# Optimization experiments

Hardware: AMD Instinct MI355X
Metric: run time of the kernel (lower is better)

Reference implementation:

```python
import jax, jax.numpy as jnp
import numpy as np

TV, B, V = 2048, 16, 1024
TK, K = 2048, 1024


def setup_inputs() -> dict:
    key = jax.random.key(0)
    k1, k2, k3 = jax.random.split(key, 3)
    values = jax.random.normal(k1, (TV, B, V), dtype=jnp.float32)          # time-major values
    values_mask = jnp.ones((B, TV), dtype=jnp.int32)                        # unused by math, kept for fidelity
    keys = jax.random.normal(k2, (B, TK, K), dtype=jnp.float32)
    # xavier-normal-scaled projection weight (created inside torch forward)
    w = jax.random.normal(k3, (K, V), dtype=jnp.float32) * jnp.sqrt(2.0 / (K + V))
    return {"values": values, "values_mask": values_mask, "keys": keys, "w": w}


def reference(values, values_mask, keys, w):
    # values: [Tv, B, V] -> values_t: [B, V, Tv]
    values_t = jnp.transpose(values, (1, 2, 0))
    # project keys: [B, Tk, K] @ [K, V] -> [B, Tk, V] (original loops per batch; vectorized here)
    part_logits = jnp.einsum('btk,kv->btv', keys, w)
    # attn logits: [B, Tk, Tv]
    attn_logits = jnp.einsum('btv,bvs->bts', part_logits, values_t)
    attn_dist = jax.nn.softmax(attn_logits, axis=-1)
    # output: [B, Tk, Tv] @ [B, Tv, V] -> [B, Tk, V]
    output = jnp.einsum('bts,bsv->btv', attn_dist, jnp.transpose(values, (1, 0, 2)))
    return attn_dist, output
```

## Files before the change

kernel.cpp:

```cpp
#include <hip/hip_runtime.h>

#define TV_ 2048
#define NB_ 16
#define NV_ 1024
#define TK_ 2048
#define NK_ 1024

typedef float    f32x4 __attribute__((ext_vector_type(4)));
typedef float    fl4   __attribute__((ext_vector_type(4)));
typedef _Float16 hfx8  __attribute__((ext_vector_type(8)));

static __device__ __forceinline__ ushort f2h(float f){
  _Float16 h = (_Float16)f;
  return __builtin_bit_cast(ushort, h);
}

__global__ __launch_bounds__(256) void cvt_h_k(const float* __restrict__ x,
                                               ushort* __restrict__ y, long n4){
  long i = (long)blockIdx.x*256 + threadIdx.x;
  const long stride = (long)gridDim.x*256;
  for (; i < n4; i += stride){
    fl4 v = ((const fl4*)x)[i];
    ((ushort4*)y)[i] = make_ushort4(f2h(v[0]), f2h(v[1]), f2h(v[2]), f2h(v[3]));
  }
}

__global__ void wtrans_k(const float* __restrict__ w, ushort* __restrict__ wT){
  __shared__ float t[32][33];
  const int tx = threadIdx.x, ty = threadIdx.y;
  const int k0 = blockIdx.x*32, v0 = blockIdx.y*32;
#pragma unroll
  for (int r=0;r<4;++r) t[ty+8*r][tx] = w[(long)(k0+ty+8*r)*NV_ + v0+tx];
  __syncthreads();
#pragma unroll
  for (int r=0;r<4;++r)
    wT[(long)(v0+ty+8*r)*NK_ + k0+tx] = f2h(t[tx][ty+8*r]);
}

__global__ void vboth_k(const float* __restrict__ vals,
                        ushort* __restrict__ v2, ushort* __restrict__ vbt){
  __shared__ float t[32][33];
  const int tx = threadIdx.x, ty = threadIdx.y;
  const int s0 = blockIdx.x*32, v0 = blockIdx.y*32, b = blockIdx.z;
#pragma unroll
  for (int r=0;r<4;++r){
    float x = vals[((long)(s0+ty+8*r)*NB_ + b)*NV_ + v0+tx];
    t[ty+8*r][tx] = x;
    v2[((long)b*TV_ + s0+ty+8*r)*NV_ + v0+tx] = f2h(x);
  }
  __syncthreads();
#pragma unroll
  for (int r=0;r<4;++r)
    vbt[((long)b*NV_ + v0+ty+8*r)*TV_ + s0+tx] = f2h(t[tx][ty+8*r]);
}

static __device__ __forceinline__ hfx8 ldfrag(const ushort* base, int r, int q){
  const int off = r*128 + (((q ^ (r & 7)) & 7) << 4);
  return *(const hfx8*)((const char*)base + off);
}

#define SAOFF(b,h) (((b)*2+(h))*8192)
#define SBOFF(b,h) (32768 + ((b)*2+(h))*8192)

#define STAGE(Xp, hb, t, ldsoff) do { \
  _Pragma("unroll") \
  for (int c_=0;c_<2;++c_) \
    __builtin_amdgcn_global_load_lds( \
      (const __attribute__((address_space(1))) unsigned*)((Xp) + (long)(hb)*128*K + (long)(t)*64 + soff[c_]), \
      (__attribute__((address_space(3))) unsigned*)(lds + (ldsoff) + chunk0[c_]*8), 16, 0, 0); \
} while(0)

#define VM4 asm volatile("s_waitcnt vmcnt(4)" ::: "memory")
#define VM0 asm volatile("s_waitcnt vmcnt(0)" ::: "memory")
#define NOPS (void)0

#define BARR() do { __builtin_amdgcn_s_barrier(); __builtin_amdgcn_sched_barrier(0); } while(0)

#define MFMA_SET(IB, JB, BREG) \
  _Pragma("unroll") for (int kk=0;kk<2;++kk) \
  _Pragma("unroll") for (int i=0;i<4;++i) \
  _Pragma("unroll") for (int j=0;j<2;++j) \
    acc[(IB)+i][(JB)+j] = __builtin_amdgcn_mfma_f32_16x16x32_f16(aR[i][kk], BREG[j][kk], acc[(IB)+i][(JB)+j], 0,0,0)

#define KTILE(BUF, S0, S1, S2, S3, EW) do { \
  const ushort* sa_ = lds + SAOFF(BUF, wr); \
  const ushort* sb_ = lds + SBOFF(BUF, (wc>>1)); \
  const int brow_ = (wc&1)*64; \
   \
  _Pragma("unroll") for (int i=0;i<4;++i) _Pragma("unroll") for (int kk=0;kk<2;++kk) \
    aR[i][kk] = ldfrag(sa_, i*16+lm, lq+kk*4); \
  _Pragma("unroll") for (int j=0;j<2;++j) _Pragma("unroll") for (int kk=0;kk<2;++kk) \
    b01[j][kk] = ldfrag(sb_, brow_ + j*16 + lm, lq+kk*4); \
  S0; \
  BARR(); \
  __builtin_amdgcn_s_setprio(1); \
  MFMA_SET(0, 0, b01); \
  __builtin_amdgcn_s_setprio(0); \
  BARR(); \
   \
  _Pragma("unroll") for (int j=0;j<2;++j) _Pragma("unroll") for (int kk=0;kk<2;++kk) \
    b23[j][kk] = ldfrag(sb_, brow_ + (2+j)*16 + lm, lq+kk*4); \
  S1; \
  BARR(); \
  __builtin_amdgcn_s_setprio(1); \
  MFMA_SET(0, 2, b23); \
  __builtin_amdgcn_s_setprio(0); \
  BARR(); \
   \
  _Pragma("unroll") for (int i=0;i<4;++i) _Pragma("unroll") for (int kk=0;kk<2;++kk) \
    aR[i][kk] = ldfrag(sa_, (4+i)*16+lm, lq+kk*4); \
  S2; \
  BARR(); \
  __builtin_amdgcn_s_setprio(1); \
  MFMA_SET(4, 2, b23); \
  __builtin_amdgcn_s_setprio(0); \
  BARR(); \
   \
  S3; \
  BARR(); \
  __builtin_amdgcn_s_setprio(1); \
  MFMA_SET(4, 0, b01); \
  __builtin_amdgcn_s_setprio(0); \
  EW; \
  BARR(); \
} while(0)

template<int OUTF16>
__global__ __launch_bounds__(512, 2)
void gemm8_k(const ushort* __restrict__ A, const ushort* __restrict__ BT,
             float* __restrict__ C, ushort* __restrict__ Ch,
             int N, int K, long sA, long sB, long sC)
{
  extern __shared__ ushort lds[];

  const int tid  = threadIdx.x;
  const int lane = tid & 63;
  const int w    = tid >> 6;
  const int wr   = w >> 2;
  const int wc   = w & 3;
  const int lm   = lane & 15, lq = lane >> 4;
  const int bz   = blockIdx.z;
  const long m0  = (long)blockIdx.y * 256;
  const long n0  = (long)blockIdx.x * 256;

  const ushort* Ap = A  + (long)bz*sA + m0*K;
  const ushort* Bp = BT + (long)bz*sB + n0*K;

  int chunk0[2], soff[2];
#pragma unroll
  for (int c=0;c<2;++c){
    chunk0[c] = (w<<7) + (c<<6);
    const int idx = chunk0[c] + lane;
    const int row = idx >> 3, sl = idx & 7;
    soff[c] = row*K + ((sl ^ (row & 7)) << 3);
  }

  f32x4 acc[8][4];
#pragma unroll
  for (int i=0;i<8;++i)
#pragma unroll
    for (int j=0;j<4;++j) acc[i][j] = (f32x4){0.f,0.f,0.f,0.f};

  hfx8 aR[4][2], b01[2][2], b23[2][2];

  const int NT = K >> 6;

  STAGE(Ap, 0, 0, SAOFF(0,0));
  STAGE(Ap, 1, 0, SAOFF(0,1));
  STAGE(Bp, 0, 0, SBOFF(0,0));
  STAGE(Bp, 1, 0, SBOFF(0,1));
  STAGE(Bp, 0, 1, SBOFF(1,0));
  STAGE(Ap, 0, 1, SAOFF(1,0));
  VM4;
  BARR();

  for (int u=0; u <= NT-4; u+=2){
    KTILE(0,
          STAGE(Ap, 1, u+1, SAOFF(1,1)),
          STAGE(Bp, 1, u+1, SBOFF(1,1)),
          STAGE(Bp, 0, u+2, SBOFF(0,0)),
          STAGE(Ap, 0, u+2, SAOFF(0,0)),
          VM4);
    KTILE(1,
          STAGE(Ap, 1, u+2, SAOFF(0,1)),
          STAGE(Bp, 1, u+2, SBOFF(0,1)),
          STAGE(Bp, 0, u+3, SBOFF(1,0)),
          STAGE(Ap, 0, u+3, SAOFF(1,0)),
          VM4);
  }
  KTILE(0,
        STAGE(Ap, 1, NT-1, SAOFF(1,1)),
        STAGE(Bp, 1, NT-1, SBOFF(1,1)),
        NOPS, NOPS, VM0);
  KTILE(1, NOPS, NOPS, NOPS, NOPS, NOPS);

  const long cb = (long)bz*sC;
#pragma unroll
  for (int i=0;i<8;++i)
#pragma unroll
    for (int j=0;j<4;++j)
#pragma unroll
      for (int g=0; g<4; ++g){
        const long gm = m0 + wr*128 + i*16 + lq*4 + g;
        const long gn = n0 + wc*64  + j*16 + lm;
        const long o = cb + gm*N + gn;
        if constexpr (OUTF16) Ch[o] = f2h(acc[i][j][g]);
        else                  C[o]  = acc[i][j][g];
      }
}

__global__ __launch_bounds__(256) void softmax_k(float* __restrict__ lg, ushort* __restrict__ pb){
  const long base = (long)blockIdx.x * TV_;
  const int tid = threadIdx.x;
  const int lane = tid & 63, w = tid >> 6;
  float x[8];
  fl4 a = *(const fl4*)(lg + base + tid*8);
  fl4 b = *(const fl4*)(lg + base + tid*8 + 4);
  x[0]=a[0];x[1]=a[1];x[2]=a[2];x[3]=a[3];x[4]=b[0];x[5]=b[1];x[6]=b[2];x[7]=b[3];
  float m = x[0];
#pragma unroll
  for (int j=1;j<8;++j) m = fmaxf(m, x[j]);
#pragma unroll
  for (int off=32; off; off>>=1) m = fmaxf(m, __shfl_xor(m, off));
  __shared__ float rm[4], rs[4];
  if (lane==0) rm[w]=m;
  __syncthreads();
  m = fmaxf(fmaxf(rm[0],rm[1]), fmaxf(rm[2],rm[3]));
  float s = 0.f;
#pragma unroll
  for (int j=0;j<8;++j){ x[j] = __expf(x[j]-m); s += x[j]; }
#pragma unroll
  for (int off=32; off; off>>=1) s += __shfl_xor(s, off);
  if (lane==0) rs[w]=s;
  __syncthreads();
  s = rs[0]+rs[1]+rs[2]+rs[3];
  const float inv = 1.f/s;
  fl4 p0 = {x[0]*inv, x[1]*inv, x[2]*inv, x[3]*inv};
  fl4 p1 = {x[4]*inv, x[5]*inv, x[6]*inv, x[7]*inv};
  *(fl4*)(lg + base + tid*8)     = p0;
  *(fl4*)(lg + base + tid*8 + 4) = p1;
  *(ushort4*)(pb + base + tid*8)     = make_ushort4(f2h(p0[0]),f2h(p0[1]),f2h(p0[2]),f2h(p0[3]));
  *(ushort4*)(pb + base + tid*8 + 4) = make_ushort4(f2h(p1[0]),f2h(p1[1]),f2h(p1[2]),f2h(p1[3]));
}

extern "C" void kernel_launch(void* const* d_in, const int* in_sizes, int n_in,
                              void* d_out, int out_size, void* d_ws, size_t ws_size,
                              hipStream_t stream){
  (void)in_sizes; (void)n_in; (void)out_size; (void)ws_size;
  const float* values = (const float*)d_in[0];
  const float* keys   = (const float*)d_in[2];
  const float* w      = (const float*)d_in[3];

  float* attn = (float*)d_out;
  float* outp = (float*)d_out + (long)NB_*TK_*TV_;

  char* ws = (char*)d_ws;
  const long MB = 1024L*1024L;
  ushort* kh  = (ushort*)(ws);
  ushort* vbt = (ushort*)(ws + 64*MB);
  ushort* plh = (ushort*)(ws + 128*MB);
  ushort* adb = (ushort*)(ws + 128*MB);
  ushort* wth = (ushort*)(ws + 256*MB);
  ushort* v2  = kh;

  const size_t LDSB = 131072;

  cvt_h_k<<<2048,256,0,stream>>>(keys, kh, (long)NB_*TK_*NK_/4);
  wtrans_k<<<dim3(32,32),dim3(32,8),0,stream>>>(w, wth);
  gemm8_k<1><<<dim3(NV_/256, TK_/256, NB_),512,LDSB,stream>>>(
      kh, wth, nullptr, plh, NV_, NK_, (long)TK_*NK_, 0L, (long)TK_*NV_);
  vboth_k<<<dim3(TV_/32, NV_/32, NB_),dim3(32,8),0,stream>>>(values, v2, vbt);
  gemm8_k<0><<<dim3(TV_/256, TK_/256, NB_),512,LDSB,stream>>>(
      plh, v2, attn, nullptr, TV_, NV_, (long)TK_*NV_, (long)TV_*NV_, (long)TK_*TV_);
  softmax_k<<<NB_*TK_,256,0,stream>>>(attn, adb);
  gemm8_k<0><<<dim3(NV_/256, TK_/256, NB_),512,LDSB,stream>>>(
      adb, vbt, outp, nullptr, NV_, TV_, (long)TK_*TV_, (long)NV_*TV_, (long)TK_*NV_);
}
```

Measured before the change: 608.5 us.

## Fuse softmax into logits GEMM epilogue and PV GEMM A-operand load

The logits GEMM epilogue now emits per-tile row max and sum-of-exp partials, and a small kernel reduces them to a per-row max and inverse sum. The PV GEMM then reads fp32 logits directly, applies exp and normalization while staging the A tile into LDS as fp16, and only the first N-block writes the fp32 attention output. This removes the standalone softmax pass and its fp16 probability buffer, at the cost of recomputing exp in each of the four N-blocks and reading fp32 logits. The path is gated on workspace size being at least 460 MB and falls back to the old path otherwise.

```diff
diff --git a/kernel.cpp b/kernel.cpp
--- a/kernel.cpp
+++ b/kernel.cpp
@@ -125,10 +125,11 @@
   BARR(); \
 } while(0)
 
-template<int OUTF16>
+template<int OUTF16, int SMPART>
 __global__ __launch_bounds__(512, 2)
 void gemm8_k(const ushort* __restrict__ A, const ushort* __restrict__ BT,
              float* __restrict__ C, ushort* __restrict__ Ch,
+             float* __restrict__ pm, float* __restrict__ ps,
              int N, int K, long sA, long sB, long sC)
 {
   extern __shared__ ushort lds[];
@@ -194,6 +195,27 @@
         NOPS, NOPS, VM0);
   KTILE(1, NOPS, NOPS, NOPS, NOPS, NOPS);
 
+  if constexpr (SMPART){
+#pragma unroll
+    for (int i=0;i<8;++i)
+#pragma unroll
+      for (int g=0; g<4; ++g){
+        float mt = fmaxf(fmaxf(acc[i][0][g], acc[i][1][g]), fmaxf(acc[i][2][g], acc[i][3][g]));
+#pragma unroll
+        for (int off=1; off<16; off<<=1) mt = fmaxf(mt, __shfl_xor(mt, off));
+        float se = 0.f;
+#pragma unroll
+        for (int j=0;j<4;++j) se += __expf(acc[i][j][g] - mt);
+#pragma unroll
+        for (int off=1; off<16; off<<=1) se += __shfl_xor(se, off);
+        if (lm == 0){
+          const long rg = (long)bz*TK_ + m0 + wr*128 + i*16 + lq*4 + g;
+          pm[rg*32 + blockIdx.x*4 + wc] = mt;
+          ps[rg*32 + blockIdx.x*4 + wc] = se;
+        }
+      }
+  }
+
   const long cb = (long)bz*sC;
 #pragma unroll
   for (int i=0;i<8;++i)
@@ -206,6 +228,144 @@
         const long o = cb + gm*N + gn;
         if constexpr (OUTF16) Ch[o] = f2h(acc[i][j][g]);
         else                  C[o]  = acc[i][j][g];
+      }
+}
+
+__global__ __launch_bounds__(256) void rs_k(const float* __restrict__ pm,
+                                            const float* __restrict__ ps,
+                                            float* __restrict__ mrow,
+                                            float* __restrict__ isrow){
+  const long r = (long)blockIdx.x*256 + threadIdx.x;
+  float m = -3.4e38f;
+#pragma unroll
+  for (int p=0;p<32;++p) m = fmaxf(m, pm[r*32+p]);
+  float s = 0.f;
+#pragma unroll
+  for (int p=0;p<32;++p) s += ps[r*32+p] * __expf(pm[r*32+p] - m);
+  mrow[r] = m;
+  isrow[r] = 1.f/s;
+}
+
+#define LDA(h, t) do { \
+  _Pragma("unroll") for (int c_=0;c_<4;++c_) \
+    aSt[c_] = *(const fl4*)(Alg + ((long)((h)*128 + arow[c_]))*TV_ + (long)(t)*64 + acol4[c_]*4); \
+} while(0)
+
+#define WRA(h, t, ldso) do { \
+  _Pragma("unroll") for (int c_=0;c_<4;++c_){ \
+    fl4 pf; \
+    _Pragma("unroll") for (int q_=0;q_<4;++q_) \
+      pf[q_] = __expf(aSt[c_][q_] - mreg[(h)*4+c_]) * isreg[(h)*4+c_]; \
+    if constexpr (WR) \
+      *(fl4*)(Pat + ((long)((h)*128 + arow[c_]))*TV_ + (long)(t)*64 + acol4[c_]*4) = pf; \
+    const int slot_ = acol4[c_] >> 1; \
+    const int bo_ = arow[c_]*128 + (((slot_ ^ (arow[c_] & 7)) & 7) << 4) + (acol4[c_] & 1)*8; \
+    *(ushort4*)((char*)lds + (long)(ldso)*2 + bo_) = \
+        make_ushort4(f2h(pf[0]), f2h(pf[1]), f2h(pf[2]), f2h(pf[3])); \
+  } \
+  asm volatile("s_waitcnt lgkmcnt(0)" ::: "memory"); \
+} while(0)
+
+#define PVS1(t, sbo, sao) do { STAGE(Bp, 1, t, sbo); WRA(1, t, sao); } while(0)
+#define PVS2(t, sbo)      do { LDA(0, t); STAGE(Bp, 0, t, sbo); } while(0)
+#define PVS3(t, sao)      do { WRA(0, t, sao); } while(0)
+
+template<int WR>
+__global__ __launch_bounds__(512, 2)
+void pv_fused_k(const float* __restrict__ lgits, const ushort* __restrict__ vbt,
+                const float* __restrict__ mrow, const float* __restrict__ isrow,
+                float* __restrict__ attn, float* __restrict__ outp, int n0off)
+{
+  extern __shared__ ushort lds[];
+
+  const int tid  = threadIdx.x;
+  const int lane = tid & 63;
+  const int w    = tid >> 6;
+  const int wr   = w >> 2;
+  const int wc   = w & 3;
+  const int lm   = lane & 15, lq = lane >> 4;
+  const int bz   = blockIdx.z;
+  const long m0  = (long)blockIdx.y * 256;
+  const long n0  = (long)(blockIdx.x + n0off) * 256;
+  const int K    = TV_;
+  const int NT   = K >> 6;
+
+  const float*  Alg = lgits + (long)bz*TK_*TV_ + m0*TV_;
+  float*        Pat = attn  + (long)bz*TK_*TV_ + m0*TV_;
+  const ushort* Bp  = vbt   + (long)bz*NV_*TV_ + n0*TV_;
+
+  int chunk0[2], soff[2];
+#pragma unroll
+  for (int c=0;c<2;++c){
+    chunk0[c] = (w<<7) + (c<<6);
+    const int idx = chunk0[c] + lane;
+    const int row = idx >> 3, sl = idx & 7;
+    soff[c] = row*K + ((sl ^ (row & 7)) << 3);
+  }
+  int arow[4], acol4[4];
+#pragma unroll
+  for (int c=0;c<4;++c){
+    const int idx = (w<<8) + (c<<6) + lane;
+    arow[c]  = idx >> 4;
+    acol4[c] = idx & 15;
+  }
+  float mreg[8], isreg[8];
+#pragma unroll
+  for (int h=0;h<2;++h)
+#pragma unroll
+    for (int c=0;c<4;++c){
+      const long rg = (long)bz*TK_ + m0 + h*128 + arow[c];
+      mreg[h*4+c]  = mrow[rg];
+      isreg[h*4+c] = isrow[rg];
+    }
+
+  f32x4 acc[8][4];
+#pragma unroll
+  for (int i=0;i<8;++i)
+#pragma unroll
+    for (int j=0;j<4;++j) acc[i][j] = (f32x4){0.f,0.f,0.f,0.f};
+
+  hfx8 aR[4][2], b01[2][2], b23[2][2];
+  fl4  aSt[4];
+
+  LDA(0,0); WRA(0,0, SAOFF(0,0));
+  LDA(1,0); WRA(1,0, SAOFF(0,1));
+  STAGE(Bp, 0, 0, SBOFF(0,0));
+  STAGE(Bp, 1, 0, SBOFF(0,1));
+  LDA(0,1); WRA(0,1, SAOFF(1,0));
+  STAGE(Bp, 0, 1, SBOFF(1,0));
+  BARR();
+
+  for (int u=0; u <= NT-4; u+=2){
+    KTILE(0,
+          LDA(1, u+1),
+          PVS1(u+1, SBOFF(1,1), SAOFF(1,1)),
+          PVS2(u+2, SBOFF(0,0)),
+          PVS3(u+2, SAOFF(0,0)),
+          NOPS);
+    KTILE(1,
+          LDA(1, u+2),
+          PVS1(u+2, SBOFF(0,1), SAOFF(0,1)),
+          PVS2(u+3, SBOFF(1,0)),
+          PVS3(u+3, SAOFF(1,0)),
+          NOPS);
+  }
+  KTILE(0,
+        LDA(1, NT-1),
+        PVS1(NT-1, SBOFF(1,1), SAOFF(1,1)),
+        NOPS, NOPS, VM0);
+  KTILE(1, NOPS, NOPS, NOPS, NOPS, NOPS);
+
+  const long cb = (long)bz*TK_*NV_;
+#pragma unroll
+  for (int i=0;i<8;++i)
+#pragma unroll
+    for (int j=0;j<4;++j)
+#pragma unroll
+      for (int g=0; g<4; ++g){
+        const long gm = m0 + wr*128 + i*16 + lq*4 + g;
+        const long gn = n0 + wc*64  + j*16 + lm;
+        outp[cb + gm*NV_ + gn] = acc[i][j][g];
       }
 }
 
@@ -246,7 +406,7 @@
 extern "C" void kernel_launch(void* const* d_in, const int* in_sizes, int n_in,
                               void* d_out, int out_size, void* d_ws, size_t ws_size,
                               hipStream_t stream){
-  (void)in_sizes; (void)n_in; (void)out_size; (void)ws_size;
+  (void)in_sizes; (void)n_in; (void)out_size;
   const float* values = (const float*)d_in[0];
   const float* keys   = (const float*)d_in[2];
   const float* w      = (const float*)d_in[3];
@@ -256,23 +416,45 @@
 
   char* ws = (char*)d_ws;
   const long MB = 1024L*1024L;
-  ushort* kh  = (ushort*)(ws);
-  ushort* vbt = (ushort*)(ws + 64*MB);
-  ushort* plh = (ushort*)(ws + 128*MB);
-  ushort* adb = (ushort*)(ws + 128*MB);
-  ushort* wth = (ushort*)(ws + 256*MB);
-  ushort* v2  = kh;
+  const bool fused = ws_size >= (size_t)(460*MB);
+
+  ushort* kh   = (ushort*)(ws);
+  ushort* vbt  = (ushort*)(ws + 64*MB);
+  ushort* plh  = (ushort*)(ws + 128*MB);
+  ushort* adb  = (ushort*)(ws + 128*MB);
+  float*  lgts = (float*)(ws + 192*MB);
+  ushort* wth  = (ushort*)(ws + (fused ? 448 : 256)*MB);
+  float*  pm   = (float*)(ws + 450*MB);
+  float*  psum = (float*)(ws + 454*MB);
+  float*  mrow = (float*)(ws + 458*MB);
+  float*  isrw = (float*)(ws + 458*MB + 256*1024);
+  ushort* v2   = kh;
 
   const size_t LDSB = 131072;
 
   cvt_h_k<<<2048,256,0,stream>>>(keys, kh, (long)NB_*TK_*NK_/4);
   wtrans_k<<<dim3(32,32),dim3(32,8),0,stream>>>(w, wth);
-  gemm8_k<1><<<dim3(NV_/256, TK_/256, NB_),512,LDSB,stream>>>(
-      kh, wth, nullptr, plh, NV_, NK_, (long)TK_*NK_, 0L, (long)TK_*NV_);
+  gemm8_k<1,0><<<dim3(NV_/256, TK_/256, NB_),512,LDSB,stream>>>(
+      kh, wth, nullptr, plh, nullptr, nullptr,
+      NV_, NK_, (long)TK_*NK_, 0L, (long)TK_*NV_);
   vboth_k<<<dim3(TV_/32, NV_/32, NB_),dim3(32,8),0,stream>>>(values, v2, vbt);
-  gemm8_k<0><<<dim3(TV_/256, TK_/256, NB_),512,LDSB,stream>>>(
-      plh, v2, attn, nullptr, TV_, NV_, (long)TK_*NV_, (long)TV_*NV_, (long)TK_*TV_);
-  softmax_k<<<NB_*TK_,256,0,stream>>>(attn, adb);
-  gemm8_k<0><<<dim3(NV_/256, TK_/256, NB_),512,LDSB,stream>>>(
-      adb, vbt, outp, nullptr, NV_, TV_, (long)TK_*TV_, (long)NV_*TV_, (long)TK_*NV_);
-}
+
+  if (fused){
+    gemm8_k<0,1><<<dim3(TV_/256, TK_/256, NB_),512,LDSB,stream>>>(
+        plh, v2, lgts, nullptr, pm, psum,
+        TV_, NV_, (long)TK_*NV_, (long)TV_*NV_, (long)TK_*TV_);
+    rs_k<<<NB_*TK_/256,256,0,stream>>>(pm, psum, mrow, isrw);
+    pv_fused_k<1><<<dim3(1, TK_/256, NB_),512,LDSB,stream>>>(
+        lgts, vbt, mrow, isrw, attn, outp, 0);
+    pv_fused_k<0><<<dim3(3, TK_/256, NB_),512,LDSB,stream>>>(
+        lgts, vbt, mrow, isrw, attn, outp, 1);
+  } else {
+    gemm8_k<0,0><<<dim3(TV_/256, TK_/256, NB_),512,LDSB,stream>>>(
+        plh, v2, attn, nullptr, nullptr, nullptr,
+        TV_, NV_, (long)TK_*NV_, (long)TV_*NV_, (long)TK_*TV_);
+    softmax_k<<<NB_*TK_,256,0,stream>>>(attn, adb);
+    gemm8_k<0,0><<<dim3(NV_/256, TK_/256, NB_),512,LDSB,stream>>>(
+        adb, vbt, outp, nullptr, nullptr, nullptr,
+        NV_, TV_, (long)TK_*TV_, (long)NV_*TV_, (long)TK_*NV_);
+  }
+}
```

New measurement: 1.353 ms. 2.22x slower.

## Fuse softmax partial statistics into logits GEMM epilogue and remap block grid

Applied to the files above, without the earlier changes.

The logits GEMM epilogue now computes per-tile row max and exp-sum and stores max-shifted logits as fp16, so the fp32 logits are never written and re-read. A small kernel combines the 32 partials per row into a log-sum-exp offset, and an elementwise kernel writes the fp32 attention and the fp16 probabilities. This removes a full fp32 read-modify-write pass over the attention matrix. In exchange, the logits pass through fp16 before exponentiation, which loses precision. The GEMM blocks are also launched on a flat 1D grid remapped to interleave tiles across XCDs. The fused path runs only when the workspace is at least 340 MB.

```diff
diff --git a/kernel.cpp b/kernel.cpp
--- a/kernel.cpp
+++ b/kernel.cpp
@@ -9,10 +9,14 @@
 typedef float    f32x4 __attribute__((ext_vector_type(4)));
 typedef float    fl4   __attribute__((ext_vector_type(4)));
 typedef _Float16 hfx8  __attribute__((ext_vector_type(8)));
+typedef ushort   us8   __attribute__((ext_vector_type(8)));
 
 static __device__ __forceinline__ ushort f2h(float f){
   _Float16 h = (_Float16)f;
   return __builtin_bit_cast(ushort, h);
+}
+static __device__ __forceinline__ float h2f(ushort u){
+  return (float)__builtin_bit_cast(_Float16, u);
 }
 
 __global__ __launch_bounds__(256) void cvt_h_k(const float* __restrict__ x,
@@ -70,8 +74,8 @@
       (__attribute__((address_space(3))) unsigned*)(lds + (ldsoff) + chunk0[c_]*8), 16, 0, 0); \
 } while(0)
 
-#define VM4 asm volatile("s_waitcnt vmcnt(4)" ::: "memory")
-#define VM0 asm volatile("s_waitcnt vmcnt(0)" ::: "memory")
+#define VM4  asm volatile("s_waitcnt vmcnt(4)"  ::: "memory")
+#define VM0  asm volatile("s_waitcnt vmcnt(0)"  ::: "memory")
 #define NOPS (void)0
 
 #define BARR() do { __builtin_amdgcn_s_barrier(); __builtin_amdgcn_sched_barrier(0); } while(0)
@@ -125,10 +129,11 @@
   BARR(); \
 } while(0)
 
-template<int OUTF16>
+template<int OUTMODE, int GXL>
 __global__ __launch_bounds__(512, 2)
 void gemm8_k(const ushort* __restrict__ A, const ushort* __restrict__ BT,
              float* __restrict__ C, ushort* __restrict__ Ch,
+             float* __restrict__ pm, float* __restrict__ ps,
              int N, int K, long sA, long sB, long sC)
 {
   extern __shared__ ushort lds[];
@@ -139,9 +144,14 @@
   const int wr   = w >> 2;
   const int wc   = w & 3;
   const int lm   = lane & 15, lq = lane >> 4;
-  const int bz   = blockIdx.z;
-  const long m0  = (long)blockIdx.y * 256;
-  const long n0  = (long)blockIdx.x * 256;
+
+  const int bid     = blockIdx.x;
+  const int logical = (bid & 7)*((int)gridDim.x >> 3) + (bid >> 3);
+  const int bx      = logical & ((1<<GXL)-1);
+  const int by      = (logical >> GXL) & 7;
+  const int bz      = logical >> (GXL+3);
+  const long m0     = (long)by * 256;
+  const long n0     = (long)bx * 256;
 
   const ushort* Ap = A  + (long)bz*sA + m0*K;
   const ushort* Bp = BT + (long)bz*sB + n0*K;
@@ -195,18 +205,91 @@
   KTILE(1, NOPS, NOPS, NOPS, NOPS, NOPS);
 
   const long cb = (long)bz*sC;
-#pragma unroll
-  for (int i=0;i<8;++i)
-#pragma unroll
-    for (int j=0;j<4;++j)
+  if constexpr (OUTMODE == 2){
+#pragma unroll
+    for (int i=0;i<8;++i){
+      float mts[4];
 #pragma unroll
       for (int g=0; g<4; ++g){
-        const long gm = m0 + wr*128 + i*16 + lq*4 + g;
-        const long gn = n0 + wc*64  + j*16 + lm;
-        const long o = cb + gm*N + gn;
-        if constexpr (OUTF16) Ch[o] = f2h(acc[i][j][g]);
-        else                  C[o]  = acc[i][j][g];
+        float mt = fmaxf(fmaxf(acc[i][0][g], acc[i][1][g]), fmaxf(acc[i][2][g], acc[i][3][g]));
+#pragma unroll
+        for (int off=1; off<16; off<<=1) mt = fmaxf(mt, __shfl_xor(mt, off));
+        float se = 0.f;
+#pragma unroll
+        for (int j=0;j<4;++j) se += __expf(acc[i][j][g] - mt);
+#pragma unroll
+        for (int off=1; off<16; off<<=1) se += __shfl_xor(se, off);
+        if (lm == 0){
+          const long rg = (long)bz*TK_ + m0 + wr*128 + i*16 + lq*4 + g;
+          pm[rg*32 + bx*4 + wc] = mt;
+          ps[rg*32 + bx*4 + wc] = se;
+        }
+        mts[g] = mt;
       }
+#pragma unroll
+      for (int j=0;j<4;++j)
+#pragma unroll
+        for (int g=0; g<4; ++g){
+          const long gm = m0 + wr*128 + i*16 + lq*4 + g;
+          const long gn = n0 + wc*64  + j*16 + lm;
+          Ch[cb + gm*N + gn] = f2h(acc[i][j][g] - mts[g]);
+        }
+    }
+  } else {
+#pragma unroll
+    for (int i=0;i<8;++i)
+#pragma unroll
+      for (int j=0;j<4;++j)
+#pragma unroll
+        for (int g=0; g<4; ++g){
+          const long gm = m0 + wr*128 + i*16 + lq*4 + g;
+          const long gn = n0 + wc*64  + j*16 + lm;
+          const long o = cb + gm*N + gn;
+          if constexpr (OUTMODE == 1) Ch[o] = f2h(acc[i][j][g]);
+          else                        C[o]  = acc[i][j][g];
+        }
+  }
+}
+
+__global__ __launch_bounds__(256) void rs_k(const float* __restrict__ pm,
+                                            const float* __restrict__ ps,
+                                            float* __restrict__ dsh2){
+  const long r = (long)blockIdx.x*256 + threadIdx.x;
+  float pmv[32];
+  float m = -3.4e38f;
+#pragma unroll
+  for (int p=0;p<32;++p){ pmv[p] = pm[r*32+p]; m = fmaxf(m, pmv[p]); }
+  float s = 0.f;
+#pragma unroll
+  for (int p=0;p<32;++p) s += ps[r*32+p] * __expf(pmv[p] - m);
+  const float lg = __logf(s);
+#pragma unroll
+  for (int p=0;p<32;++p) dsh2[r*32+p] = pmv[p] - m - lg;
+}
+
+__global__ __launch_bounds__(256) void pexp_k(const ushort* __restrict__ h16,
+                                              const float* __restrict__ dsh2,
+                                              float* __restrict__ attn,
+                                              ushort* __restrict__ p16){
+  const long n8 = (long)NB_*TK_*TV_/8;
+  long i = (long)blockIdx.x*256 + threadIdx.x;
+  const long stride = (long)gridDim.x*256;
+  for (; i < n8; i += stride){
+    us8 hv = ((const us8*)h16)[i];
+    const long row = i >> 8;
+    const int  c8  = (int)(i & 255);
+    const float d = dsh2[row*32 + (c8>>3)];
+    float p[8];
+#pragma unroll
+    for (int e=0;e<8;++e) p[e] = __expf(h2f((ushort)hv[e]) + d);
+    fl4 q0 = {p[0],p[1],p[2],p[3]}, q1 = {p[4],p[5],p[6],p[7]};
+    *(fl4*)(attn + i*8)     = q0;
+    *(fl4*)(attn + i*8 + 4) = q1;
+    us8 o;
+#pragma unroll
+    for (int e=0;e<8;++e) o[e] = f2h(p[e]);
+    ((us8*)p16)[i] = o;
+  }
 }
 
 __global__ __launch_bounds__(256) void softmax_k(float* __restrict__ lg, ushort* __restrict__ pb){
@@ -246,7 +329,7 @@
 extern "C" void kernel_launch(void* const* d_in, const int* in_sizes, int n_in,
                               void* d_out, int out_size, void* d_ws, size_t ws_size,
                               hipStream_t stream){
-  (void)in_sizes; (void)n_in; (void)out_size; (void)ws_size;
+  (void)in_sizes; (void)n_in; (void)out_size;
   const float* values = (const float*)d_in[0];
   const float* keys   = (const float*)d_in[2];
   const float* w      = (const float*)d_in[3];
@@ -256,23 +339,56 @@
 
   char* ws = (char*)d_ws;
   const long MB = 1024L*1024L;
-  ushort* kh  = (ushort*)(ws);
-  ushort* vbt = (ushort*)(ws + 64*MB);
-  ushort* plh = (ushort*)(ws + 128*MB);
-  ushort* adb = (ushort*)(ws + 128*MB);
-  ushort* wth = (ushort*)(ws + 256*MB);
-  ushort* v2  = kh;
-
+  const bool fused = ws_size >= (size_t)(340*MB);
   const size_t LDSB = 131072;
 
-  cvt_h_k<<<2048,256,0,stream>>>(keys, kh, (long)NB_*TK_*NK_/4);
-  wtrans_k<<<dim3(32,32),dim3(32,8),0,stream>>>(w, wth);
-  gemm8_k<1><<<dim3(NV_/256, TK_/256, NB_),512,LDSB,stream>>>(
-      kh, wth, nullptr, plh, NV_, NK_, (long)TK_*NK_, 0L, (long)TK_*NV_);
-  vboth_k<<<dim3(TV_/32, NV_/32, NB_),dim3(32,8),0,stream>>>(values, v2, vbt);
-  gemm8_k<0><<<dim3(TV_/256, TK_/256, NB_),512,LDSB,stream>>>(
-      plh, v2, attn, nullptr, TV_, NV_, (long)TK_*NV_, (long)TV_*NV_, (long)TK_*TV_);
-  softmax_k<<<NB_*TK_,256,0,stream>>>(attn, adb);
-  gemm8_k<0><<<dim3(NV_/256, TK_/256, NB_),512,LDSB,stream>>>(
-      adb, vbt, outp, nullptr, NV_, TV_, (long)TK_*TV_, (long)NV_*TV_, (long)TK_*NV_);
-}
+  if (fused){
+    ushort* kh   = (ushort*)(ws);
+    ushort* vbt  = (ushort*)(ws + 64*MB);
+    ushort* plh  = (ushort*)(ws + 128*MB);
+    ushort* adb  = (ushort*)(ws + 192*MB);
+    float*  pm   = (float*)(ws + 320*MB);
+    float*  psum = (float*)(ws + 324*MB);
+    float*  dsh2 = (float*)(ws + 328*MB);
+    ushort* wth  = (ushort*)(ws + 332*MB);
+    ushort* v2   = kh;
+    ushort* p16  = plh;
+    p16 = adb;
+
+    cvt_h_k<<<2048,256,0,stream>>>(keys, kh, (long)NB_*TK_*NK_/4);
+    wtrans_k<<<dim3(32,32),dim3(32,8),0,stream>>>(w, wth);
+    gemm8_k<1,2><<<512,512,LDSB,stream>>>(
+        kh, wth, nullptr, plh, nullptr, nullptr,
+        NV_, NK_, (long)TK_*NK_, 0L, (long)TK_*NV_);
+    vboth_k<<<dim3(TV_/32, NV_/32, NB_),dim3(32,8),0,stream>>>(values, v2, vbt);
+    gemm8_k<2,3><<<1024,512,LDSB,stream>>>(
+        plh, v2, nullptr, adb, pm, psum,
+        TV_, NV_, (long)TK_*NV_, (long)TV_*NV_, (long)TK_*TV_);
+    rs_k<<<NB_*TK_/256,256,0,stream>>>(pm, psum, dsh2);
+    pexp_k<<<2048,256,0,stream>>>(adb, dsh2, attn, p16);
+    gemm8_k<0,2><<<512,512,LDSB,stream>>>(
+        p16, vbt, outp, nullptr, nullptr, nullptr,
+        NV_, TV_, (long)TK_*TV_, (long)NV_*TV_, (long)TK_*NV_);
+  } else {
+    ushort* kh  = (ushort*)(ws);
+    ushort* vbt = (ushort*)(ws + 64*MB);
+    ushort* plh = (ushort*)(ws + 128*MB);
+    ushort* adb = (ushort*)(ws + 128*MB);
+    ushort* wth = (ushort*)(ws + 256*MB);
+    ushort* v2  = kh;
+
+    cvt_h_k<<<2048,256,0,stream>>>(keys, kh, (long)NB_*TK_*NK_/4);
+    wtrans_k<<<dim3(32,32),dim3(32,8),0,stream>>>(w, wth);
+    gemm8_k<1,2><<<512,512,LDSB,stream>>>(
+        kh, wth, nullptr, plh, nullptr, nullptr,
+        NV_, NK_, (long)TK_*NK_, 0L, (long)TK_*NV_);
+    vboth_k<<<dim3(TV_/32, NV_/32, NB_),dim3(32,8),0,stream>>>(values, v2, vbt);
+    gemm8_k<0,3><<<1024,512,LDSB,stream>>>(
+        plh, v2, attn, nullptr, nullptr, nullptr,
+        TV_, NV_, (long)TK_*NV_, (long)TV_*NV_, (long)TK_*TV_);
+    softmax_k<<<NB_*TK_,256,0,stream>>>(attn, adb);
+    gemm8_k<0,2><<<512,512,LDSB,stream>>>(
+        adb, vbt, outp, nullptr, nullptr, nullptr,
+        NV_, TV_, (long)TK_*TV_, (long)NV_*TV_, (long)TK_*NV_);
+  }
+}
```

Result: no change. 608.5 us (+0.0%).
